# Performance work log

Measured on AMD Instinct MI355X. Metric: run time of the kernel, lower is better.

Reference implementation:

```python
import jax, jax.numpy as jnp
import numpy as np

B, L, D, H1, OUT, MAX_W = 16, 128, 768, 770, 40, 30


def _span_mask():
    # valid spans: i <= j and width < MAX_W (structured sparsity over the L x L grid)
    ii, jj = np.meshgrid(np.arange(L), np.arange(L), indexing='ij')
    return ((jj >= ii) & (jj - ii < MAX_W)).astype(np.int32)


def setup_inputs():
    key = jax.random.key(0)
    ks = jax.random.split(key, 5)
    hidden_states = jax.random.normal(ks[0], (B, L + 1, D), dtype=jnp.float32)
    rng = np.random.default_rng(0)
    starts = rng.integers(0, L - MAX_W, size=(B,))
    ends = starts + rng.integers(0, MAX_W, size=(B,))
    pred_spans = jnp.asarray(np.stack([starts, ends], axis=1), dtype=jnp.int32)
    span_mask = jnp.asarray(_span_mask())
    W1 = 0.02 * jax.random.normal(ks[1], (2 * D + 1, H1), dtype=jnp.float32)
    b1 = jax.random.normal(ks[2], (H1,), dtype=jnp.float32)
    W2 = 0.02 * jax.random.normal(ks[3], (H1, OUT), dtype=jnp.float32)
    b2 = jax.random.normal(ks[4], (OUT,), dtype=jnp.float32)
    return dict(hidden_states=hidden_states, pred_spans=pred_spans, token_num=L,
                span_available_indication_matrix=span_mask,
                W1=W1, b1=b1, W2=W2, b2=b2)


def reference(hidden_states, pred_spans, token_num, span_available_indication_matrix, W1, b1, W2, b2):
    # span mask is an integer constant -> resolve valid (i, j) pairs on host
    mask = np.asarray(span_available_indication_matrix)
    vi, vj = np.nonzero(mask == 1)            # [n_valid] each
    vi_j = jnp.asarray(vi)
    vj_j = jnp.asarray(vj)
    vecs = hidden_states[:, 1:token_num + 1, :]  # token t -> hidden[:, t+1, :], [B, L, D]
    xi = vecs[:, vi_j, :]                        # [B, n_valid, D] gather of span-start vecs
    xj = vecs[:, vj_j, :]                        # [B, n_valid, D] gather of span-end vecs
    # pred_indications: 2 if span == pred span; 1 if strictly inside it (i<=j); else 0
    s = pred_spans[:, 0:1]
    e = pred_spans[:, 1:2]
    i_ = vi_j[None, :]
    j_ = vj_j[None, :]
    exact = (i_ == s) & (j_ == e)
    inside = (i_ >= s) & (j_ <= e) & (i_ <= j_)
    ind = jnp.where(exact, 2.0, jnp.where(inside, 1.0, 0.0)).astype(hidden_states.dtype)  # [B, n_valid]
    # Linear over concat([xi, xj, ind]) expressed as split matmuls (avoids materializing concat)
    W1i, W1j, w1c = W1[:D], W1[D:2 * D], W1[2 * D]
    h = (jnp.einsum('bnd,dh->bnh', xi, W1i)
         + jnp.einsum('bnd,dh->bnh', xj, W1j)
         + ind[..., None] * w1c + b1)
    h = jax.nn.relu(h)
    logits = jnp.einsum('bnh,ho->bno', h, W2) + b2   # [B, n_valid, OUT]
    return jax.nn.log_softmax(logits, axis=-1)
```

## Files before the change

kernel.cpp:

```cpp
#include <hip/hip_runtime.h>
#include <math.h>

#define B_ 16
#define L_ 128
#define D_ 768
#define H1_ 770
#define OUT_ 40
#define NPAIRS 3405
#define NLOG 1540
#define YSB 1552
#define VOFFB 776
#define KPAD 800
#define W1TROWS 1600
#define NKS 25

#define NB_X 1536
#define NB_W 160
#define NB_T 1200
#define NB_A (NB_X + NB_W + NB_T)
#define NB_B 800
#define NB_C 1008

typedef __attribute__((ext_vector_type(8))) short bf16x8;
typedef __attribute__((ext_vector_type(8))) unsigned short u16x8;
typedef __attribute__((ext_vector_type(4))) float f32x4;
typedef __attribute__((ext_vector_type(4))) unsigned int u32x4;

__device__ inline unsigned short f2bf(float f) {
  unsigned int u = __builtin_bit_cast(unsigned int, f);
  u += 0x7fffu + ((u >> 16) & 1u);
  return (unsigned short)(u >> 16);
}
__device__ inline float bf2f(unsigned short x) {
  return __builtin_bit_cast(float, (unsigned int)x << 16);
}

#if __has_builtin(__builtin_amdgcn_cvt_pk_bf16_f32)
typedef __attribute__((ext_vector_type(2))) __bf16 bf16x2_t;
__device__ inline unsigned int pack_bf16(float lo, float hi) {
  bf16x2_t r = __builtin_amdgcn_cvt_pk_bf16_f32(lo, hi);
  return __builtin_bit_cast(unsigned int, r);
}
#else
__device__ inline unsigned int pack_bf16(float lo, float hi) {
  return (unsigned int)f2bf(lo) | ((unsigned int)f2bf(hi) << 16);
}
#endif

typedef const __attribute__((address_space(1))) void* gas_t;
typedef __attribute__((address_space(3))) void* las_t;
__device__ inline void gl2lds16(const void* g, void* l) {
  __builtin_amdgcn_global_load_lds((gas_t)g, (las_t)l, 16, 0, 0);
}

__device__ inline void tile_decode(int T, int& ti, int& d) {
  if (T < 216) { ti = T / 9; d = T - ti * 9; }
  else {
    int m = T - 216; int r = 24, w = 8;
    while (m >= w) { m -= w; --w; ++r; }
    ti = r; d = m;
  }
}
__device__ inline int pair_rank(int i, int j) {
  return (i < 99) ? i * 30 + (j - i)
                  : NPAIRS - (128 - i) * (129 - i) / 2 + (j - i);
}

__global__ __launch_bounds__(256) void prep_k(
    const float* __restrict__ hidden, const float* __restrict__ W1,
    const float* __restrict__ b1, const float* __restrict__ W2,
    unsigned short* __restrict__ Xb, unsigned short* __restrict__ W1T,
    unsigned short* __restrict__ Bswz, float* __restrict__ Cv)
{
  __shared__ float t[32][33];
  const int u = blockIdx.x;
  const int tid = threadIdx.x;

  if (u < NB_X) {
    int idx = u * 256 + tid;
    int m = idx / 192;
    int c = idx - m * 192;
    float4 f = *(const float4*)(hidden + (size_t)(m + (m >> 7) + 1) * D_ + c * 4);
    ushort4 o;
    o.x = f2bf(f.x); o.y = f2bf(f.y); o.z = f2bf(f.z); o.w = f2bf(f.w);
    *(ushort4*)(Xb + (size_t)m * D_ + c * 4) = o;
  } else if (u < NB_X + NB_W) {
    int idx = (u - NB_X) * 256 + tid;
    if (idx < NKS * 3 * 512) {
      int ks = idx / 1536;
      int rem = idx - ks * 1536;
      int f = rem / 512;
      int l = (rem - f * 512) >> 3;
      int e = rem & 7;
      int n = f * 16 + (l & 15);
      int k = ks * 32 + (l >> 4) * 8 + e;
      float v = (n < OUT_ && k < H1_) ? W2[k * OUT_ + n] : 0.f;
      Bswz[idx] = f2bf(v);
    } else if (idx < NKS * 3 * 512 + 3 * KPAD) {
      int c = idx - NKS * 3 * 512;
      int tt = c / KPAD, k = c - tt * KPAD;
      const float* w1c = W1 + 1536 * H1_;
      Cv[c] = (k < H1_) ? (b1[k] + (float)tt * w1c[k]) : 0.f;
    }
  } else {
    int bx = u - NB_X - NB_W;
    const int tx = tid & 31, ty = tid >> 5;
    const int n0 = (bx % 50) * 32, k0 = (bx / 50) * 32;
    #pragma unroll
    for (int r = 0; r < 4; ++r) {
      int k = k0 + ty + r * 8, n = n0 + tx;
      float v = 0.f;
      if (n < H1_)       v = W1[k * H1_ + n];
      else if (n < NLOG) v = W1[(D_ + k) * H1_ + (n - H1_)];
      t[ty + r * 8][tx] = v;
    }
    __syncthreads();
    #pragma unroll
    for (int r = 0; r < 4; ++r) {
      int n = n0 + ty + r * 8, k = k0 + tx;
      W1T[(size_t)n * D_ + k] = f2bf(t[tx][ty + r * 8]);
    }
  }
}

__global__ __launch_bounds__(256) void gemm_k(
    const unsigned short* __restrict__ Xb, const unsigned short* __restrict__ W1T,
    unsigned short* __restrict__ Yb)
{
  __shared__ unsigned short As[64][64];
  __shared__ unsigned short Bs[64][64];
  const int tid = threadIdx.x;
  const int lane = tid & 63, w = tid >> 6;
  const int lm = lane & 15, q = lane >> 4;
  const int row0 = (blockIdx.x / 25) * 64, col0 = (blockIdx.x % 25) * 64;
  const int m0 = (w >> 1) * 32, n0 = (w & 1) * 32;

  const int srow = w * 16 + (lane >> 3);
  const int schunk = (((lane & 7) ^ ((lane >> 3) & 7))) * 8;
  const unsigned short* ga = Xb  + (size_t)(row0 + srow) * D_ + schunk;
  const unsigned short* gb = W1T + (size_t)(col0 + srow) * D_ + schunk;

  const int xs = lm & 7;

  f32x4 acc[2][2] = {};

  for (int k0 = 0; k0 < D_; k0 += 64) {
    gl2lds16(ga + k0,          &As[w * 16][0]);
    gl2lds16(ga + k0 + 8 * D_, &As[w * 16 + 8][0]);
    gl2lds16(gb + k0,          &Bs[w * 16][0]);
    gl2lds16(gb + k0 + 8 * D_, &Bs[w * 16 + 8][0]);
    __syncthreads();
    #pragma unroll
    for (int ks = 0; ks < 2; ++ks) {
      const int cc = ((ks * 4 + q) ^ xs) * 8;
      bf16x8 a0 = *(const bf16x8*)&As[m0 + lm]     [cc];
      bf16x8 a1 = *(const bf16x8*)&As[m0 + 16 + lm][cc];
      bf16x8 b0 = *(const bf16x8*)&Bs[n0 + lm]     [cc];
      bf16x8 b1 = *(const bf16x8*)&Bs[n0 + 16 + lm][cc];
      acc[0][0] = __builtin_amdgcn_mfma_f32_16x16x32_bf16(a0, b0, acc[0][0], 0, 0, 0);
      acc[0][1] = __builtin_amdgcn_mfma_f32_16x16x32_bf16(a0, b1, acc[0][1], 0, 0, 0);
      acc[1][0] = __builtin_amdgcn_mfma_f32_16x16x32_bf16(a1, b0, acc[1][0], 0, 0, 0);
      acc[1][1] = __builtin_amdgcn_mfma_f32_16x16x32_bf16(a1, b1, acc[1][1], 0, 0, 0);
    }
    __syncthreads();
  }

  #pragma unroll
  for (int ti = 0; ti < 2; ++ti) {
    #pragma unroll
    for (int tj = 0; tj < 2; ++tj) {
      int col = col0 + n0 + tj * 16 + lm;
      if (col >= NLOG) continue;
      int pc = (col < H1_) ? col : col + (VOFFB - H1_);
      #pragma unroll
      for (int r = 0; r < 4; ++r) {
        int row = row0 + m0 + ti * 16 + q * 4 + r;
        Yb[(size_t)row * YSB + pc] = f2bf(acc[ti][tj][r]);
      }
    }
  }
}

__global__ __launch_bounds__(256) void pair_k(
    const unsigned short* __restrict__ Yb, const int* __restrict__ spans,
    const unsigned short* __restrict__ Bswz, const float* __restrict__ Cv,
    const float* __restrict__ b2, float* __restrict__ out)
{
  const int tid = threadIdx.x;
  const int u = blockIdx.x;
  const int lane = tid & 63, w = tid >> 6;
  const int lm = lane & 15, q = lane >> 4;
  const int bb = u / 63;
  int ti, d;
  tile_decode((u % 63) * 4 + w, ti, d);
  const int i0 = ti * 4, j0 = (ti + d) * 4;

  const int ai = i0 + (lm & 3);
  const int aj = j0 + (lm >> 2);
  const int s = spans[2 * bb], e = spans[2 * bb + 1];
  const int ind = (ai == s && aj == e) ? 2 : ((ai >= s && aj <= e) ? 1 : 0);

  const unsigned short* uptr = Yb + (size_t)(bb * L_ + ai) * YSB + q * 8;
  const unsigned short* vptr = Yb + (size_t)(bb * L_ + aj) * YSB + VOFFB + q * 8;
  const float* cptr = Cv + ind * KPAD + q * 8;
  const unsigned short* bbase = Bswz + lane * 8;

  f32x4 acc0 = {}, acc1 = {}, acc2 = {};

  u16x8 uu = *(const u16x8*)(uptr);
  u16x8 vv = *(const u16x8*)(vptr);

  #pragma unroll 5
  for (int ks = 0; ks < NKS; ++ks) {
    const int ko = ks * 32;
    u16x8 cu = uu, cw = vv;
    uu = *(const u16x8*)(uptr + ko + 32);
    vv = *(const u16x8*)(vptr + ko + 32);
    float4 c0 = *(const float4*)(cptr + ko);
    float4 c1 = *(const float4*)(cptr + ko + 4);
    float h0 = fmaxf(bf2f(cu[0]) + bf2f(cw[0]) + c0.x, 0.f);
    float h1 = fmaxf(bf2f(cu[1]) + bf2f(cw[1]) + c0.y, 0.f);
    float h2 = fmaxf(bf2f(cu[2]) + bf2f(cw[2]) + c0.z, 0.f);
    float h3 = fmaxf(bf2f(cu[3]) + bf2f(cw[3]) + c0.w, 0.f);
    float h4 = fmaxf(bf2f(cu[4]) + bf2f(cw[4]) + c1.x, 0.f);
    float h5 = fmaxf(bf2f(cu[5]) + bf2f(cw[5]) + c1.y, 0.f);
    float h6 = fmaxf(bf2f(cu[6]) + bf2f(cw[6]) + c1.z, 0.f);
    float h7 = fmaxf(bf2f(cu[7]) + bf2f(cw[7]) + c1.w, 0.f);
    u32x4 hp;
    hp[0] = pack_bf16(h0, h1);
    hp[1] = pack_bf16(h2, h3);
    hp[2] = pack_bf16(h4, h5);
    hp[3] = pack_bf16(h6, h7);
    bf16x8 a = __builtin_bit_cast(bf16x8, hp);
    bf16x8 bf0 = *(const bf16x8*)(bbase + (size_t)(ks * 3 + 0) * 512);
    bf16x8 bf1 = *(const bf16x8*)(bbase + (size_t)(ks * 3 + 1) * 512);
    bf16x8 bf2v = *(const bf16x8*)(bbase + (size_t)(ks * 3 + 2) * 512);
    acc0 = __builtin_amdgcn_mfma_f32_16x16x32_bf16(a, bf0, acc0, 0, 0, 0);
    acc1 = __builtin_amdgcn_mfma_f32_16x16x32_bf16(a, bf1, acc1, 0, 0, 0);
    acc2 = __builtin_amdgcn_mfma_f32_16x16x32_bf16(a, bf2v, acc2, 0, 0, 0);
  }

  const float b2v0 = b2[lm];
  const float b2v1 = b2[16 + lm];
  const float b2v2 = (lm < 8) ? b2[32 + lm] : 0.f;

  #pragma unroll
  for (int r = 0; r < 4; ++r) {
    float l0 = acc0[r] + b2v0;
    float l1 = acc1[r] + b2v1;
    float l2 = (lm < 8) ? (acc2[r] + b2v2) : -INFINITY;
    float mx = fmaxf(fmaxf(l0, l1), l2);
    mx = fmaxf(mx, __shfl_xor(mx, 1));
    mx = fmaxf(mx, __shfl_xor(mx, 2));
    mx = fmaxf(mx, __shfl_xor(mx, 4));
    mx = fmaxf(mx, __shfl_xor(mx, 8));
    float sm = expf(l0 - mx) + expf(l1 - mx) + ((lm < 8) ? expf(l2 - mx) : 0.f);
    sm += __shfl_xor(sm, 1);
    sm += __shfl_xor(sm, 2);
    sm += __shfl_xor(sm, 4);
    sm += __shfl_xor(sm, 8);
    float lsd = mx + logf(sm);

    int pi_ = i0 + r, pj_ = j0 + q;
    if (pj_ >= pi_ && (pj_ - pi_) < 30) {
      float* op = out + ((size_t)bb * NPAIRS + pair_rank(pi_, pj_)) * OUT_;
      op[lm]      = l0 - lsd;
      op[16 + lm] = l1 - lsd;
      if (lm < 8) op[32 + lm] = l2 - lsd;
    }
  }
}

extern "C" void kernel_launch(void* const* d_in, const int* in_sizes, int n_in,
                              void* d_out, int out_size, void* d_ws, size_t ws_size,
                              hipStream_t stream) {
  const float* hidden = (const float*)d_in[0];
  const int*   spans  = (const int*)d_in[1];
  const float* W1 = (const float*)d_in[4];
  const float* b1 = (const float*)d_in[5];
  const float* W2 = (const float*)d_in[6];
  const float* b2 = (const float*)d_in[7];
  float* out = (float*)d_out;

  char* base = (char*)d_ws;
  size_t off = 0;
  auto take = [&](size_t bytes) {
    char* p = base + off;
    off = (off + bytes + 255) & ~(size_t)255;
    return p;
  };
  unsigned short* Yb   = (unsigned short*)take((size_t)2049 * YSB * 2);
  unsigned short* Xb   = (unsigned short*)take((size_t)2048 * D_ * 2);
  unsigned short* W1T  = (unsigned short*)take((size_t)W1TROWS * D_ * 2);
  unsigned short* Bswz = (unsigned short*)take((size_t)NKS * 3 * 512 * 2);
  float*          Cv   = (float*)take((size_t)3 * KPAD * 4);

  prep_k<<<dim3(NB_A), 256, 0, stream>>>(hidden, W1, b1, W2, Xb, W1T, Bswz, Cv);
  gemm_k<<<dim3(NB_B), 256, 0, stream>>>(Xb, W1T, Yb);
  pair_k<<<dim3(NB_C), 256, 0, stream>>>(Yb, spans, Bswz, Cv, b2, out);
}
```

Baseline: 121.5 us.

## Remap GEMM blocks per XCD, shrink pair blocks to one wave, deepen prefetch

The GEMM block index is remapped so that each XCD (blockIdx mod 8) handles a contiguous band of row tiles, which should improve L2 reuse of X rows. The pair kernel now launches one wave per block, with batch as the fastest block index, and prefetches Y rows two k-steps ahead and the W2 fragments one step ahead. Bswz is padded to 26 k-steps so the prefetch past the last step stays in bounds. This adds register pressure and multiplies the block count by four in exchange for better latency hiding.

After: 118.8 us (median of 2 runs). 1.02x faster.

```diff
diff --git a/kernel.cpp b/kernel.cpp
--- a/kernel.cpp
+++ b/kernel.cpp
@@ -13,13 +13,15 @@
 #define KPAD 800
 #define W1TROWS 1600
 #define NKS 25
+#define NTILES 252
+#define BSWZ_N (26 * 3 * 512)
 
 #define NB_X 1536
-#define NB_W 160
+#define NB_W 166
 #define NB_T 1200
 #define NB_A (NB_X + NB_W + NB_T)
 #define NB_B 800
-#define NB_C 1008
+#define NB_C (NTILES * 16)
 
 typedef __attribute__((ext_vector_type(8))) short bf16x8;
 typedef __attribute__((ext_vector_type(8))) unsigned short u16x8;
@@ -86,7 +88,7 @@
     *(ushort4*)(Xb + (size_t)m * D_ + c * 4) = o;
   } else if (u < NB_X + NB_W) {
     int idx = (u - NB_X) * 256 + tid;
-    if (idx < NKS * 3 * 512) {
+    if (idx < BSWZ_N) {
       int ks = idx / 1536;
       int rem = idx - ks * 1536;
       int f = rem / 512;
@@ -96,8 +98,8 @@
       int k = ks * 32 + (l >> 4) * 8 + e;
       float v = (n < OUT_ && k < H1_) ? W2[k * OUT_ + n] : 0.f;
       Bswz[idx] = f2bf(v);
-    } else if (idx < NKS * 3 * 512 + 3 * KPAD) {
-      int c = idx - NKS * 3 * 512;
+    } else if (idx < BSWZ_N + 3 * KPAD) {
+      int c = idx - BSWZ_N;
       int tt = c / KPAD, k = c - tt * KPAD;
       const float* w1c = W1 + 1536 * H1_;
       Cv[c] = (k < H1_) ? (b1[k] + (float)tt * w1c[k]) : 0.f;
@@ -132,7 +134,10 @@
   const int tid = threadIdx.x;
   const int lane = tid & 63, w = tid >> 6;
   const int lm = lane & 15, q = lane >> 4;
-  const int row0 = (blockIdx.x / 25) * 64, col0 = (blockIdx.x % 25) * 64;
+  const int xcd = blockIdx.x & 7;
+  const int t = blockIdx.x >> 3;
+  const int col0 = (t % 25) * 64;
+  const int row0 = (xcd * 4 + t / 25) * 64;
   const int m0 = (w >> 1) * 32, n0 = (w & 1) * 32;
 
   const int srow = w * 16 + (lane >> 3);
@@ -181,18 +186,19 @@
   }
 }
 
-__global__ __launch_bounds__(256) void pair_k(
+__global__ __launch_bounds__(64) void pair_k(
     const unsigned short* __restrict__ Yb, const int* __restrict__ spans,
     const unsigned short* __restrict__ Bswz, const float* __restrict__ Cv,
     const float* __restrict__ b2, float* __restrict__ out)
 {
   const int tid = threadIdx.x;
   const int u = blockIdx.x;
-  const int lane = tid & 63, w = tid >> 6;
-  const int lm = lane & 15, q = lane >> 4;
-  const int bb = u / 63;
+  const int bb = u & 15;
+  const int T = u >> 4;
+  const int lm = tid & 15, q = tid >> 4;
+
   int ti, d;
-  tile_decode((u % 63) * 4 + w, ti, d);
+  tile_decode(T, ti, d);
   const int i0 = ti * 4, j0 = (ti + d) * 4;
 
   const int ai = i0 + (lm & 3);
@@ -203,19 +209,29 @@
   const unsigned short* uptr = Yb + (size_t)(bb * L_ + ai) * YSB + q * 8;
   const unsigned short* vptr = Yb + (size_t)(bb * L_ + aj) * YSB + VOFFB + q * 8;
   const float* cptr = Cv + ind * KPAD + q * 8;
-  const unsigned short* bbase = Bswz + lane * 8;
+  const unsigned short* bbase = Bswz + tid * 8;
 
   f32x4 acc0 = {}, acc1 = {}, acc2 = {};
 
-  u16x8 uu = *(const u16x8*)(uptr);
-  u16x8 vv = *(const u16x8*)(vptr);
+  u16x8 uu0 = *(const u16x8*)(uptr);
+  u16x8 vv0 = *(const u16x8*)(vptr);
+  u16x8 uu1 = *(const u16x8*)(uptr + 32);
+  u16x8 vv1 = *(const u16x8*)(vptr + 32);
+  bf16x8 nb0 = *(const bf16x8*)(bbase + 0 * 512);
+  bf16x8 nb1 = *(const bf16x8*)(bbase + 1 * 512);
+  bf16x8 nb2 = *(const bf16x8*)(bbase + 2 * 512);
 
   #pragma unroll 5
   for (int ks = 0; ks < NKS; ++ks) {
     const int ko = ks * 32;
-    u16x8 cu = uu, cw = vv;
-    uu = *(const u16x8*)(uptr + ko + 32);
-    vv = *(const u16x8*)(vptr + ko + 32);
+    u16x8 cu = uu0, cw = vv0;
+    uu0 = uu1; vv0 = vv1;
+    uu1 = *(const u16x8*)(uptr + ko + 64);
+    vv1 = *(const u16x8*)(vptr + ko + 64);
+    bf16x8 b0 = nb0, b1v = nb1, b2f = nb2;
+    nb0 = *(const bf16x8*)(bbase + (size_t)(ks * 3 + 3) * 512);
+    nb1 = *(const bf16x8*)(bbase + (size_t)(ks * 3 + 4) * 512);
+    nb2 = *(const bf16x8*)(bbase + (size_t)(ks * 3 + 5) * 512);
     float4 c0 = *(const float4*)(cptr + ko);
     float4 c1 = *(const float4*)(cptr + ko + 4);
     float h0 = fmaxf(bf2f(cu[0]) + bf2f(cw[0]) + c0.x, 0.f);
@@ -232,12 +248,9 @@
     hp[2] = pack_bf16(h4, h5);
     hp[3] = pack_bf16(h6, h7);
     bf16x8 a = __builtin_bit_cast(bf16x8, hp);
-    bf16x8 bf0 = *(const bf16x8*)(bbase + (size_t)(ks * 3 + 0) * 512);
-    bf16x8 bf1 = *(const bf16x8*)(bbase + (size_t)(ks * 3 + 1) * 512);
-    bf16x8 bf2v = *(const bf16x8*)(bbase + (size_t)(ks * 3 + 2) * 512);
-    acc0 = __builtin_amdgcn_mfma_f32_16x16x32_bf16(a, bf0, acc0, 0, 0, 0);
-    acc1 = __builtin_amdgcn_mfma_f32_16x16x32_bf16(a, bf1, acc1, 0, 0, 0);
-    acc2 = __builtin_amdgcn_mfma_f32_16x16x32_bf16(a, bf2v, acc2, 0, 0, 0);
+    acc0 = __builtin_amdgcn_mfma_f32_16x16x32_bf16(a, b0, acc0, 0, 0, 0);
+    acc1 = __builtin_amdgcn_mfma_f32_16x16x32_bf16(a, b1v, acc1, 0, 0, 0);
+    acc2 = __builtin_amdgcn_mfma_f32_16x16x32_bf16(a, b2f, acc2, 0, 0, 0);
   }
 
   const float b2v0 = b2[lm];
@@ -292,10 +305,10 @@
   unsigned short* Yb   = (unsigned short*)take((size_t)2049 * YSB * 2);
   unsigned short* Xb   = (unsigned short*)take((size_t)2048 * D_ * 2);
   unsigned short* W1T  = (unsigned short*)take((size_t)W1TROWS * D_ * 2);
-  unsigned short* Bswz = (unsigned short*)take((size_t)NKS * 3 * 512 * 2);
+  unsigned short* Bswz = (unsigned short*)take((size_t)BSWZ_N * 2);
   float*          Cv   = (float*)take((size_t)3 * KPAD * 4);
 
   prep_k<<<dim3(NB_A), 256, 0, stream>>>(hidden, W1, b1, W2, Xb, W1T, Bswz, Cv);
   gemm_k<<<dim3(NB_B), 256, 0, stream>>>(Xb, W1T, Yb);
-  pair_k<<<dim3(NB_C), 256, 0, stream>>>(Yb, spans, Bswz, Cv, b2, out);
-}
+  pair_k<<<dim3(NB_C), 64, 0, stream>>>(Yb, spans, Bswz, Cv, b2, out);
+}
```
